# Kernel tuning notes

Measured on AMD Instinct MI355X. Metric: run time of the kernel, lower is better.

## Reference

```python
import jax, jax.numpy as jnp
import numpy as np

SEQ_LEN, N_FEAT, EMB = 512, 8, 64
HID = 2 * EMB  # 128
BATCH = 512


def _lstm_layer(x, Wih, Whh, bih, bhh):
    """Single-layer LSTM, batch_first x: [B,T,F]. PyTorch gate order i,f,g,o.
    Returns (outputs [B,T,H], final hidden [B,H])."""
    B = x.shape[0]
    H = Whh.shape[1]
    # precompute input projections for all timesteps: [B,T,4H]
    xp = jnp.einsum('btf,gf->btg', x, Wih) + bih + bhh

    def step(carry, xt):
        h, c = carry
        gates = xt + h @ Whh.T  # [B,4H]
        i, f, g, o = jnp.split(gates, 4, axis=-1)
        i = jax.nn.sigmoid(i)
        f = jax.nn.sigmoid(f)
        g = jnp.tanh(g)
        o = jax.nn.sigmoid(o)
        c = f * c + i * g
        h = o * jnp.tanh(c)
        return (h, c), h

    h0 = jnp.zeros((B, H), dtype=x.dtype)
    c0 = jnp.zeros((B, H), dtype=x.dtype)
    (hT, _), hs = jax.lax.scan(step, (h0, c0), xp.transpose(1, 0, 2))
    return hs.transpose(1, 0, 2), hT


def setup_inputs() -> dict:
    key = jax.random.key(0)
    ks = jax.random.split(key, 13)
    inp = {"x": jax.random.normal(ks[0], (BATCH, SEQ_LEN, N_FEAT), dtype=jnp.float32)}

    def mk(k, shape, fan):
        s = 1.0 / np.sqrt(fan)
        return jax.random.uniform(k, shape, dtype=jnp.float32, minval=-s, maxval=s)

    # layer 1: in=N_FEAT, hid=HID
    inp["Wih1"] = mk(ks[1], (4 * HID, N_FEAT), HID)
    inp["Whh1"] = mk(ks[2], (4 * HID, HID), HID)
    inp["bih1"] = mk(ks[3], (4 * HID,), HID)
    inp["bhh1"] = mk(ks[4], (4 * HID,), HID)
    # layer 2: in=HID, hid=HID
    inp["Wih2"] = mk(ks[5], (4 * HID, HID), HID)
    inp["Whh2"] = mk(ks[6], (4 * HID, HID), HID)
    inp["bih2"] = mk(ks[7], (4 * HID,), HID)
    inp["bhh2"] = mk(ks[8], (4 * HID,), HID)
    # layer 3: in=HID, hid=EMB
    inp["Wih3"] = mk(ks[9], (4 * EMB, HID), EMB)
    inp["Whh3"] = mk(ks[10], (4 * EMB, EMB), EMB)
    inp["bih3"] = mk(ks[11], (4 * EMB,), EMB)
    inp["bhh3"] = mk(ks[12], (4 * EMB,), EMB)
    return inp


def reference(x, Wih1, Whh1, bih1, bhh1, Wih2, Whh2, bih2, bhh2, Wih3, Whh3, bih3, bhh3):
    B = x.shape[0]
    x = x.reshape(B, SEQ_LEN, N_FEAT)
    x, _ = _lstm_layer(x, Wih1, Whh1, bih1, bhh1)
    x, _ = _lstm_layer(x, Wih2, Whh2, bih2, bhh2)
    _, hT = _lstm_layer(x, Wih3, Whh3, bih3, bhh3)
    return hT  # [B, EMB]
```

## Files before the change

kernel.cpp:

```cpp
#include <hip/hip_runtime.h>


#define DEVI __device__ __forceinline__

typedef _Float16 h4 __attribute__((ext_vector_type(4)));
typedef _Float16 h8 __attribute__((ext_vector_type(8)));
typedef float f4 __attribute__((ext_vector_type(4)));

static constexpr int T_ = 512, TC_ = 16, NC_ = T_ / TC_, RC_ = 4;
static constexpr float KS_ = -1.44269504f;
static constexpr float KG_ = -2.88539008f;

DEVI float rcpf_(float x) { return __builtin_amdgcn_rcpf(x); }
DEVI float exp2f_(float x) { return __builtin_amdgcn_exp2f(x); }

DEVI h8 cvt8s(const float* p, float s) {
    const float4 a = *reinterpret_cast<const float4*>(p);
    const float4 b = *reinterpret_cast<const float4*>(p + 4);
    return h8{(_Float16)(a.x * s), (_Float16)(a.y * s), (_Float16)(a.z * s), (_Float16)(a.w * s),
              (_Float16)(b.x * s), (_Float16)(b.y * s), (_Float16)(b.z * s), (_Float16)(b.w * s)};
}

DEVI void lds_barrier() {
    asm volatile("s_waitcnt lgkmcnt(0)\n\ts_barrier" ::: "memory");
}
DEVI int ld_flag(int* f) {
    return __hip_atomic_load(f, __ATOMIC_RELAXED, __HIP_MEMORY_SCOPE_AGENT);
}
DEVI void st_flag(int* f, int v) {
    __hip_atomic_store(f, v, __ATOMIC_RELAXED, __HIP_MEMORY_SCOPE_AGENT);
}

#define POINTWISE_PROLOG(ACC)                                                   \
    float e0[4], e1[4], e2[4], e3[4];                                           \
    _Pragma("unroll") for (int i = 0; i < 4; i++) {                             \
        e0[i] = exp2f_(ACC[0][i]);                                              \
        e1[i] = exp2f_(ACC[1][i]);                                              \
        e2[i] = exp2f_(ACC[2][i]);                                              \
        e3[i] = exp2f_(ACC[3][i]); }

#define POINTWISE_CELL(i, C, HVAR)                                              \
    const float gi = rcpf_(1.f + e0[i]), gf = rcpf_(1.f + e1[i]);               \
    const float gg = 2.f * rcpf_(1.f + e2[i]) - 1.f, go = rcpf_(1.f + e3[i]);   \
    C[i] = gf * C[i] + gi * gg;                                                 \
    const float HVAR = go * (2.f * rcpf_(1.f + exp2f_(C[i] * KG_)) - 1.f);

DEVI float gscale(int q) { return (q == 2) ? KG_ : KS_; }

DEVI void stage_L1(int tile, char* smem, const float* x, const float* Wih,
                   const float* Whh, const float* bih, const float* bhh,
                   _Float16* o1, int* c1, int* p1) {
    constexpr int H = 128, KT_H = 4, HP = H + 8;
    const int tid = threadIdx.x, lane = tid & 63, wv = tid >> 6;
    const int lr = lane & 15, lk = lane >> 4;
    const int b0 = tile * 16;
    const int jcol = wv * 16 + lr;
    _Float16 (*h_lds)[16][HP] = (_Float16 (*)[16][HP])smem;

    h8 wbh[4][KT_H], wbx[4];
    float bias[4];
#pragma unroll
    for (int q = 0; q < 4; q++) {
        const float s = gscale(q);
#pragma unroll
        for (int kt = 0; kt < KT_H; kt++)
            wbh[q][kt] = cvt8s(Whh + (size_t)(q * H + jcol) * H + kt * 32 + lk * 8, s);
        wbx[q] = (lk == 0) ? cvt8s(Wih + (size_t)(q * H + jcol) * 8, s) : h8{};
        bias[q] = (bih[q * H + jcol] + bhh[q * H + jcol]) * s;
    }
    float c[4] = {0.f, 0.f, 0.f, 0.f};
    for (int i = tid; i < 2 * 16 * HP; i += 512) ((_Float16*)smem)[i] = (_Float16)0;
    __syncthreads();

    auto load_x = [&](int t, h8& xa) {
        if (lk == 0) xa = cvt8s(x + ((size_t)(b0 + lr) * T_ + t) * 8, 1.f);
    };
    h8 xa = h8{}, xb = h8{};

#define L1_STEP(TT, CUR, XS) {                                                  \
    const int tt = (TT);                                                        \
    h8 ha[KT_H];                                                                \
    _Pragma("unroll") for (int kt = 0; kt < KT_H; kt++)                         \
        ha[kt] = *reinterpret_cast<const h8*>(&h_lds[CUR][lr][kt * 32 + lk * 8]); \
    f4 acc[4];                                                                  \
    _Pragma("unroll") for (int q = 0; q < 4; q++)                               \
        acc[q] = f4{bias[q], bias[q], bias[q], bias[q]};                        \
    _Pragma("unroll") for (int q = 0; q < 4; q++)                               \
        acc[q] = __builtin_amdgcn_mfma_f32_16x16x32_f16(XS, wbx[q], acc[q], 0, 0, 0); \
    _Pragma("unroll") for (int kt = 0; kt < KT_H; kt++)                         \
        _Pragma("unroll") for (int q = 0; q < 4; q++)                           \
            acc[q] = __builtin_amdgcn_mfma_f32_16x16x32_f16(ha[kt], wbh[q][kt], acc[q], 0, 0, 0); \
    if (tt + 2 < TC_) load_x(t0 + tt + 2, XS);                                  \
    POINTWISE_PROLOG(acc)                                                       \
    _Pragma("unroll") for (int i = 0; i < 4; i++) {                             \
        POINTWISE_CELL(i, c, h)                                                 \
        const int row = lk * 4 + i;                                             \
        h_lds[(CUR) ^ 1][row][jcol] = (_Float16)h;                              \
        o1[(((size_t)(tile * RC_ + slot) * TC_ + tt) * 16 + row) * 128 + jcol] = (_Float16)h; } }

    for (int ch = 0; ch < NC_; ch++) {
        const int slot = ch & (RC_ - 1);
        if (tid == 0) {
            while (ld_flag(c1) < ch - (RC_ - 1)) __builtin_amdgcn_s_sleep(8);
        }
        __syncthreads();
        const int t0 = ch * TC_;
        load_x(t0, xa); load_x(t0 + 1, xb);
        for (int tb = 0; tb < TC_ / 2; tb++) {
            L1_STEP(2 * tb, 0, xa) lds_barrier();
            L1_STEP(2 * tb + 1, 1, xb) lds_barrier();
        }
        asm volatile("s_waitcnt vmcnt(0)" ::: "memory");
        __syncthreads();
        if (tid == 0) { __threadfence(); st_flag(p1, ch + 1); }
    }
#undef L1_STEP
}

DEVI void stage_P2(int tile, const _Float16* o1, _Float16* xp, const float* Wih,
                   const float* bih, const float* bhh,
                   int* p1, int* c1, int* cx, int* px) {
    constexpr int H = 128;
    const int tid = threadIdx.x, lane = tid & 63, wv = tid >> 6;
    const int lr = lane & 15, lk = lane >> 4;
    const int jcol = wv * 16 + lr;

    h8 wbx[4][4];
    float pbias[4];
#pragma unroll
    for (int q = 0; q < 4; q++) {
        const float s = gscale(q);
#pragma unroll
        for (int kt = 0; kt < 4; kt++)
            wbx[q][kt] = cvt8s(Wih + (size_t)(q * H + jcol) * 128 + kt * 32 + lk * 8, s);
        pbias[q] = (bih[q * H + jcol] + bhh[q * H + jcol]) * s;
    }

    for (int ch = 0; ch < NC_; ch++) {
        const int slot = ch & (RC_ - 1);
        if (tid == 0) {
            while (ld_flag(p1) < ch + 1) __builtin_amdgcn_s_sleep(8);
            while (ld_flag(cx) < ch - (RC_ - 1)) __builtin_amdgcn_s_sleep(8);
            __threadfence();
        }
        __syncthreads();
        const size_t ib = (size_t)(tile * RC_ + slot) * TC_ * 2048;
        const size_t ob = (size_t)(tile * RC_ + slot) * TC_ * 8192;
#pragma unroll 4
        for (int t = 0; t < TC_; t++) {
            h8 af[4];
#pragma unroll
            for (int kt = 0; kt < 4; kt++)
                af[kt] = *reinterpret_cast<const h8*>(o1 + ib + (size_t)t * 2048 + lr * 128 + kt * 32 + lk * 8);
            f4 acc[4];
#pragma unroll
            for (int q = 0; q < 4; q++) acc[q] = f4{pbias[q], pbias[q], pbias[q], pbias[q]};
#pragma unroll
            for (int kt = 0; kt < 4; kt++)
#pragma unroll
                for (int q = 0; q < 4; q++)
                    acc[q] = __builtin_amdgcn_mfma_f32_16x16x32_f16(af[kt], wbx[q][kt], acc[q], 0, 0, 0);
#pragma unroll
            for (int q = 0; q < 4; q++) {
                const h4 o = h4{(_Float16)acc[q][0], (_Float16)acc[q][1],
                                (_Float16)acc[q][2], (_Float16)acc[q][3]};
                *reinterpret_cast<h4*>(xp + ob + (size_t)t * 8192 + (wv * 4 + q) * 256 + lane * 4) = o;
            }
        }
        asm volatile("s_waitcnt vmcnt(0)" ::: "memory");
        __syncthreads();
        if (tid == 0) { __threadfence(); st_flag(px, ch + 1); st_flag(c1, ch + 1); }
    }
}

DEVI void stage_L2(int tile, char* smem, const _Float16* xp, _Float16* O2,
                   const float* Whh, int* px, int* cx, int* p2) {
    constexpr int H = 128, KT_H = 4, HP = H + 8;
    const int tid = threadIdx.x, lane = tid & 63, wv = tid >> 6;
    const int lr = lane & 15, lk = lane >> 4;
    const int b0 = tile * 16;
    const int jcol = wv * 16 + lr;
    _Float16 (*h_lds)[16][HP] = (_Float16 (*)[16][HP])smem;

    h8 wbh[4][KT_H];
#pragma unroll
    for (int q = 0; q < 4; q++) {
        const float s = gscale(q);
#pragma unroll
        for (int kt = 0; kt < KT_H; kt++)
            wbh[q][kt] = cvt8s(Whh + (size_t)(q * H + jcol) * H + kt * 32 + lk * 8, s);
    }
    float c[4] = {0.f, 0.f, 0.f, 0.f};
    for (int i = tid; i < 2 * 16 * HP; i += 512) ((_Float16*)smem)[i] = (_Float16)0;
    __syncthreads();

    h4 xqa[4], xqb[4];

#define LOAD_XP(SLOT, TTL, DST) {                                               \
    const size_t base = ((size_t)(tile * RC_ + (SLOT)) * TC_ + (TTL)) * 8192 + wv * 1024 + lane * 4; \
    _Pragma("unroll") for (int q = 0; q < 4; q++)                               \
        DST[q] = *reinterpret_cast<const h4*>(xp + base + q * 256); }

#define L2_STEP(TT, CUR, XQ) {                                                  \
    const int tt = (TT); const int t = t0 + tt;                                 \
    h8 ha[KT_H];                                                                \
    _Pragma("unroll") for (int kt = 0; kt < KT_H; kt++)                         \
        ha[kt] = *reinterpret_cast<const h8*>(&h_lds[CUR][lr][kt * 32 + lk * 8]); \
    f4 acc[4];                                                                  \
    _Pragma("unroll") for (int q = 0; q < 4; q++)                               \
        acc[q] = f4{(float)XQ[q][0], (float)XQ[q][1], (float)XQ[q][2], (float)XQ[q][3]}; \
    _Pragma("unroll") for (int kt = 0; kt < KT_H; kt++)                         \
        _Pragma("unroll") for (int q = 0; q < 4; q++)                           \
            acc[q] = __builtin_amdgcn_mfma_f32_16x16x32_f16(ha[kt], wbh[q][kt], acc[q], 0, 0, 0); \
    if (tt + 2 < TC_) LOAD_XP(slot, tt + 2, XQ)                                 \
    POINTWISE_PROLOG(acc)                                                       \
    _Pragma("unroll") for (int i = 0; i < 4; i++) {                             \
        POINTWISE_CELL(i, c, h)                                                 \
        const int row = lk * 4 + i;                                             \
        h_lds[(CUR) ^ 1][row][jcol] = (_Float16)h;                              \
        O2[((size_t)t * 512 + (b0 + row)) * 128 + jcol] = (_Float16)h; } }

    for (int ch = 0; ch < NC_; ch++) {
        const int slot = ch & (RC_ - 1);
        if (tid == 0) {
            while (ld_flag(px) < ch + 1) __builtin_amdgcn_s_sleep(8);
            __threadfence();
        }
        __syncthreads();
        const int t0 = ch * TC_;
        LOAD_XP(slot, 0, xqa)
        LOAD_XP(slot, 1, xqb)
        for (int tb = 0; tb < TC_ / 2; tb++) {
            L2_STEP(2 * tb, 0, xqa) lds_barrier();
            L2_STEP(2 * tb + 1, 1, xqb) lds_barrier();
        }
        asm volatile("s_waitcnt vmcnt(0)" ::: "memory");
        __syncthreads();
        if (tid == 0) { __threadfence(); st_flag(p2, ch + 1); st_flag(cx, ch + 1); }
    }
#undef L2_STEP
#undef LOAD_XP
}

DEVI void stage_L3(int tile, char* smem, const _Float16* O2, const float* Wih,
                   const float* Whh, const float* bih, const float* bhh,
                   float* out, int* p2) {
    constexpr int H = 64, KT_H = 2, KT_X = 4, HP = H + 8;
    const int tid = threadIdx.x, lane = tid & 63, wv = tid >> 6;
    const int lr = lane & 15, lk = lane >> 4;
    const int b0 = tile * 16;
    const bool act = (wv < 4);
    const int jcol = (wv & 3) * 16 + lr;
    _Float16 (*h_lds)[16][HP] = (_Float16 (*)[16][HP])smem;

    h8 wbh[4][KT_H], wbx[4][KT_X];
    float bias[4];
    if (act) {
#pragma unroll
        for (int q = 0; q < 4; q++) {
            const float s = gscale(q);
#pragma unroll
            for (int kt = 0; kt < KT_H; kt++)
                wbh[q][kt] = cvt8s(Whh + (size_t)(q * H + jcol) * H + kt * 32 + lk * 8, s);
#pragma unroll
            for (int kt = 0; kt < KT_X; kt++)
                wbx[q][kt] = cvt8s(Wih + (size_t)(q * H + jcol) * 128 + kt * 32 + lk * 8, s);
            bias[q] = (bih[q * H + jcol] + bhh[q * H + jcol]) * s;
        }
    }
    float c[4] = {0.f, 0.f, 0.f, 0.f};
    for (int i = tid; i < 2 * 16 * HP; i += 512) ((_Float16*)smem)[i] = (_Float16)0;
    __syncthreads();

    auto load_x = [&](int t, h8* xa) {
#pragma unroll
        for (int kt = 0; kt < KT_X; kt++)
            xa[kt] = *reinterpret_cast<const h8*>(
                O2 + ((size_t)t * 512 + (b0 + lr)) * 128 + kt * 32 + lk * 8);
    };
    h8 xa[KT_X], xb[KT_X];

#define L3_STEP(TT, CUR, XS) {                                                  \
    const int tt = (TT); const int t = t0 + tt;                                 \
    if (act) {                                                                  \
        h8 ha[KT_H];                                                            \
        _Pragma("unroll") for (int kt = 0; kt < KT_H; kt++)                     \
            ha[kt] = *reinterpret_cast<const h8*>(&h_lds[CUR][lr][kt * 32 + lk * 8]); \
        f4 acc[4];                                                              \
        _Pragma("unroll") for (int q = 0; q < 4; q++)                           \
            acc[q] = f4{bias[q], bias[q], bias[q], bias[q]};                    \
        _Pragma("unroll") for (int kt = 0; kt < KT_X; kt++)                     \
            _Pragma("unroll") for (int q = 0; q < 4; q++)                       \
                acc[q] = __builtin_amdgcn_mfma_f32_16x16x32_f16(XS[kt], wbx[q][kt], acc[q], 0, 0, 0); \
        _Pragma("unroll") for (int kt = 0; kt < KT_H; kt++)                     \
            _Pragma("unroll") for (int q = 0; q < 4; q++)                       \
                acc[q] = __builtin_amdgcn_mfma_f32_16x16x32_f16(ha[kt], wbh[q][kt], acc[q], 0, 0, 0); \
        if (tt + 2 < TC_) load_x(t + 2, XS);                                    \
        POINTWISE_PROLOG(acc)                                                   \
        _Pragma("unroll") for (int i = 0; i < 4; i++) {                         \
            POINTWISE_CELL(i, c, h)                                             \
            const int row = lk * 4 + i;                                         \
            h_lds[(CUR) ^ 1][row][jcol] = (_Float16)h;                          \
            if (t == T_ - 1) out[(size_t)(b0 + row) * 64 + jcol] = h; } } }

    for (int ch = 0; ch < NC_; ch++) {
        if (tid == 0) {
            while (ld_flag(p2) < ch + 1) __builtin_amdgcn_s_sleep(8);
            __threadfence();
        }
        __syncthreads();
        const int t0 = ch * TC_;
        if (act) { load_x(t0, xa); load_x(t0 + 1, xb); }
        for (int tb = 0; tb < TC_ / 2; tb++) {
            L3_STEP(2 * tb, 0, xa) lds_barrier();
            L3_STEP(2 * tb + 1, 1, xb) lds_barrier();
        }
    }
#undef L3_STEP
}

__global__ __launch_bounds__(512, 1)
void mega_k(const float* __restrict__ x,
            const float* __restrict__ Wih1, const float* __restrict__ Whh1,
            const float* __restrict__ bih1, const float* __restrict__ bhh1,
            const float* __restrict__ Wih2, const float* __restrict__ Whh2,
            const float* __restrict__ bih2, const float* __restrict__ bhh2,
            const float* __restrict__ Wih3, const float* __restrict__ Whh3,
            const float* __restrict__ bih3, const float* __restrict__ bhh3,
            _Float16* __restrict__ o1ring, _Float16* __restrict__ xpring,
            _Float16* __restrict__ O2, float* __restrict__ out,
            int* __restrict__ flags) {
    extern __shared__ char smem[];
    const int bid = blockIdx.x;
    int* p1 = flags;
    int* c1 = flags + 32;
    int* px = flags + 64;
    int* cx = flags + 96;
    int* p2 = flags + 128;
    if (bid < 32) {
        stage_L1(bid, smem, x, Wih1, Whh1, bih1, bhh1, o1ring, c1 + bid, p1 + bid);
    } else if (bid < 64) {
        const int t = bid - 32;
        stage_P2(t, o1ring, xpring, Wih2, bih2, bhh2, p1 + t, c1 + t, cx + t, px + t);
    } else if (bid < 96) {
        const int t = bid - 64;
        stage_L2(t, smem, xpring, O2, Whh2, px + t, cx + t, p2 + t);
    } else {
        const int t = bid - 96;
        stage_L3(t, smem, O2, Wih3, Whh3, bih3, bhh3, out, p2 + t);
    }
}

__global__ void zero_flags_k(int* flags) {
    if (threadIdx.x < 160)
        __hip_atomic_store(flags + threadIdx.x, 0, __ATOMIC_RELAXED,
                           __HIP_MEMORY_SCOPE_AGENT);
}

extern "C" void kernel_launch(void* const* d_in, const int* in_sizes, int n_in,
                              void* d_out, int out_size, void* d_ws, size_t ws_size,
                              hipStream_t stream) {
    const float* x = (const float*)d_in[0];
    float* out = (float*)d_out;

    char* ws = (char*)d_ws;
    _Float16* o1ring = (_Float16*)ws;
    _Float16* xpring = (_Float16*)(ws + (size_t)8388608);
    _Float16* O2     = (_Float16*)(ws + (size_t)41943040);
    int* flags       = (int*)(ws + (size_t)109051904);
    (void)ws_size; (void)in_sizes; (void)n_in; (void)out_size;

    zero_flags_k<<<1, 192, 0, stream>>>(flags);
    mega_k<<<128, 512, 8704, stream>>>(
        x,
        (const float*)d_in[1], (const float*)d_in[2], (const float*)d_in[3], (const float*)d_in[4],
        (const float*)d_in[5], (const float*)d_in[6], (const float*)d_in[7], (const float*)d_in[8],
        (const float*)d_in[9], (const float*)d_in[10], (const float*)d_in[11], (const float*)d_in[12],
        o1ring, xpring, O2, out, flags);
}
```

Before: 712.2 us.

## Process two batch tiles per block in recurrent LSTM stages

Each L1, L2 and L3 block now handles two 16-row batch tiles instead of one. L1 and L2 interleave two independent recurrences so each tile's MFMA chain can hide the other's latency. L3 puts the second tile on the four previously idle waves. The grid shrinks from 128 to 80 blocks, shared memory per block doubles, and the O2 layout changes from time-major to batch-major. The cost is a longer serial step per block and higher register pressure.

```diff
diff --git a/kernel.cpp b/kernel.cpp
--- a/kernel.cpp
+++ b/kernel.cpp
@@ -31,31 +31,30 @@
     __hip_atomic_store(f, v, __ATOMIC_RELAXED, __HIP_MEMORY_SCOPE_AGENT);
 }
 
-#define POINTWISE_PROLOG(ACC)                                                   \
+DEVI float gscale(int q) { return (q == 2) ? KG_ : KS_; }
+
+#define PW_PROLOG(A)                                                            \
     float e0[4], e1[4], e2[4], e3[4];                                           \
     _Pragma("unroll") for (int i = 0; i < 4; i++) {                             \
-        e0[i] = exp2f_(ACC[0][i]);                                              \
-        e1[i] = exp2f_(ACC[1][i]);                                              \
-        e2[i] = exp2f_(ACC[2][i]);                                              \
-        e3[i] = exp2f_(ACC[3][i]); }
-
-#define POINTWISE_CELL(i, C, HVAR)                                              \
+        e0[i] = exp2f_(A[0][i]); e1[i] = exp2f_(A[1][i]);                       \
+        e2[i] = exp2f_(A[2][i]); e3[i] = exp2f_(A[3][i]); }
+
+#define PW_CELL(i, C, HVAR)                                                     \
     const float gi = rcpf_(1.f + e0[i]), gf = rcpf_(1.f + e1[i]);               \
     const float gg = 2.f * rcpf_(1.f + e2[i]) - 1.f, go = rcpf_(1.f + e3[i]);   \
     C[i] = gf * C[i] + gi * gg;                                                 \
     const float HVAR = go * (2.f * rcpf_(1.f + exp2f_(C[i] * KG_)) - 1.f);
 
-DEVI float gscale(int q) { return (q == 2) ? KG_ : KS_; }
-
-DEVI void stage_L1(int tile, char* smem, const float* x, const float* Wih,
+DEVI void stage_L1(int tA, int tB, char* smem, const float* x, const float* Wih,
                    const float* Whh, const float* bih, const float* bhh,
                    _Float16* o1, int* c1, int* p1) {
     constexpr int H = 128, KT_H = 4, HP = H + 8;
     const int tid = threadIdx.x, lane = tid & 63, wv = tid >> 6;
     const int lr = lane & 15, lk = lane >> 4;
-    const int b0 = tile * 16;
+    const int b0A = tA * 16, b0B = tB * 16;
     const int jcol = wv * 16 + lr;
-    _Float16 (*h_lds)[16][HP] = (_Float16 (*)[16][HP])smem;
+    _Float16 (*hA)[16][HP] = (_Float16 (*)[16][HP])smem;
+    _Float16 (*hB)[16][HP] = (_Float16 (*)[16][HP])(smem + 2 * 16 * HP * 2);
 
     h8 wbh[4][KT_H], wbx[4];
     float bias[4];
@@ -68,53 +67,74 @@
         wbx[q] = (lk == 0) ? cvt8s(Wih + (size_t)(q * H + jcol) * 8, s) : h8{};
         bias[q] = (bih[q * H + jcol] + bhh[q * H + jcol]) * s;
     }
-    float c[4] = {0.f, 0.f, 0.f, 0.f};
-    for (int i = tid; i < 2 * 16 * HP; i += 512) ((_Float16*)smem)[i] = (_Float16)0;
+    float cA[4] = {0.f, 0.f, 0.f, 0.f}, cB[4] = {0.f, 0.f, 0.f, 0.f};
+    for (int i = tid; i < 2 * 2 * 16 * HP; i += 512) ((_Float16*)smem)[i] = (_Float16)0;
     __syncthreads();
 
-    auto load_x = [&](int t, h8& xa) {
+    auto load_x = [&](int b0, int t, h8& xa) {
         if (lk == 0) xa = cvt8s(x + ((size_t)(b0 + lr) * T_ + t) * 8, 1.f);
     };
-    h8 xa = h8{}, xb = h8{};
-
-#define L1_STEP(TT, CUR, XS) {                                                  \
+    h8 xAe = h8{}, xAo = h8{}, xBe = h8{}, xBo = h8{};
+
+#define L1S(TT, CUR, XA, XB) {                                                  \
     const int tt = (TT);                                                        \
-    h8 ha[KT_H];                                                                \
-    _Pragma("unroll") for (int kt = 0; kt < KT_H; kt++)                         \
-        ha[kt] = *reinterpret_cast<const h8*>(&h_lds[CUR][lr][kt * 32 + lk * 8]); \
-    f4 acc[4];                                                                  \
-    _Pragma("unroll") for (int q = 0; q < 4; q++)                               \
-        acc[q] = f4{bias[q], bias[q], bias[q], bias[q]};                        \
-    _Pragma("unroll") for (int q = 0; q < 4; q++)                               \
-        acc[q] = __builtin_amdgcn_mfma_f32_16x16x32_f16(XS, wbx[q], acc[q], 0, 0, 0); \
-    _Pragma("unroll") for (int kt = 0; kt < KT_H; kt++)                         \
-        _Pragma("unroll") for (int q = 0; q < 4; q++)                           \
-            acc[q] = __builtin_amdgcn_mfma_f32_16x16x32_f16(ha[kt], wbh[q][kt], acc[q], 0, 0, 0); \
-    if (tt + 2 < TC_) load_x(t0 + tt + 2, XS);                                  \
-    POINTWISE_PROLOG(acc)                                                       \
-    _Pragma("unroll") for (int i = 0; i < 4; i++) {                             \
-        POINTWISE_CELL(i, c, h)                                                 \
-        const int row = lk * 4 + i;                                             \
-        h_lds[(CUR) ^ 1][row][jcol] = (_Float16)h;                              \
-        o1[(((size_t)(tile * RC_ + slot) * TC_ + tt) * 16 + row) * 128 + jcol] = (_Float16)h; } }
+    h8 haA[KT_H], haB[KT_H];                                                    \
+    _Pragma("unroll") for (int kt = 0; kt < KT_H; kt++) {                       \
+        haA[kt] = *reinterpret_cast<const h8*>(&hA[CUR][lr][kt * 32 + lk * 8]); \
+        haB[kt] = *reinterpret_cast<const h8*>(&hB[CUR][lr][kt * 32 + lk * 8]); } \
+    f4 aA[4], aB[4];                                                            \
+    _Pragma("unroll") for (int q = 0; q < 4; q++) {                             \
+        aA[q] = f4{bias[q], bias[q], bias[q], bias[q]};                         \
+        aB[q] = f4{bias[q], bias[q], bias[q], bias[q]}; }                       \
+    _Pragma("unroll") for (int q = 0; q < 4; q++) {                             \
+        aA[q] = __builtin_amdgcn_mfma_f32_16x16x32_f16(XA, wbx[q], aA[q], 0, 0, 0); \
+        aB[q] = __builtin_amdgcn_mfma_f32_16x16x32_f16(XB, wbx[q], aB[q], 0, 0, 0); } \
+    _Pragma("unroll") for (int kt = 0; kt < KT_H; kt++)                         \
+        _Pragma("unroll") for (int q = 0; q < 4; q++)                           \
+            aA[q] = __builtin_amdgcn_mfma_f32_16x16x32_f16(haA[kt], wbh[q][kt], aA[q], 0, 0, 0); \
+    _Pragma("unroll") for (int kt = 0; kt < KT_H; kt++)                         \
+        _Pragma("unroll") for (int q = 0; q < 4; q++)                           \
+            aB[q] = __builtin_amdgcn_mfma_f32_16x16x32_f16(haB[kt], wbh[q][kt], aB[q], 0, 0, 0); \
+    if (tt + 2 < TC_) { load_x(b0A, t0 + tt + 2, XA); load_x(b0B, t0 + tt + 2, XB); } \
+    {                                                                           \
+        PW_PROLOG(aA)                                                           \
+        _Pragma("unroll") for (int i = 0; i < 4; i++) {                         \
+            PW_CELL(i, cA, h)                                                   \
+            const int row = lk * 4 + i;                                         \
+            hA[(CUR) ^ 1][row][jcol] = (_Float16)h;                             \
+            o1[(((size_t)(tA * RC_ + slot) * TC_ + tt) * 16 + row) * 128 + jcol] = (_Float16)h; } \
+    }                                                                           \
+    {                                                                           \
+        PW_PROLOG(aB)                                                           \
+        _Pragma("unroll") for (int i = 0; i < 4; i++) {                         \
+            PW_CELL(i, cB, h)                                                   \
+            const int row = lk * 4 + i;                                         \
+            hB[(CUR) ^ 1][row][jcol] = (_Float16)h;                             \
+            o1[(((size_t)(tB * RC_ + slot) * TC_ + tt) * 16 + row) * 128 + jcol] = (_Float16)h; } \
+    } }
 
     for (int ch = 0; ch < NC_; ch++) {
         const int slot = ch & (RC_ - 1);
         if (tid == 0) {
-            while (ld_flag(c1) < ch - (RC_ - 1)) __builtin_amdgcn_s_sleep(8);
+            while (ld_flag(c1 + tA) < ch - (RC_ - 1)) __builtin_amdgcn_s_sleep(8);
+            while (ld_flag(c1 + tB) < ch - (RC_ - 1)) __builtin_amdgcn_s_sleep(8);
         }
         __syncthreads();
         const int t0 = ch * TC_;
-        load_x(t0, xa); load_x(t0 + 1, xb);
+        load_x(b0A, t0, xAe); load_x(b0A, t0 + 1, xAo);
+        load_x(b0B, t0, xBe); load_x(b0B, t0 + 1, xBo);
         for (int tb = 0; tb < TC_ / 2; tb++) {
-            L1_STEP(2 * tb, 0, xa) lds_barrier();
-            L1_STEP(2 * tb + 1, 1, xb) lds_barrier();
+            L1S(2 * tb, 0, xAe, xBe) lds_barrier();
+            L1S(2 * tb + 1, 1, xAo, xBo) lds_barrier();
         }
         asm volatile("s_waitcnt vmcnt(0)" ::: "memory");
         __syncthreads();
-        if (tid == 0) { __threadfence(); st_flag(p1, ch + 1); }
-    }
-#undef L1_STEP
+        if (tid == 0) {
+            __threadfence();
+            st_flag(p1 + tA, ch + 1); st_flag(p1 + tB, ch + 1);
+        }
+    }
+#undef L1S
 }
 
 DEVI void stage_P2(int tile, const _Float16* o1, _Float16* xp, const float* Wih,
@@ -173,14 +193,15 @@
     }
 }
 
-DEVI void stage_L2(int tile, char* smem, const _Float16* xp, _Float16* O2,
+DEVI void stage_L2(int tA, int tB, char* smem, const _Float16* xp, _Float16* O2,
                    const float* Whh, int* px, int* cx, int* p2) {
     constexpr int H = 128, KT_H = 4, HP = H + 8;
     const int tid = threadIdx.x, lane = tid & 63, wv = tid >> 6;
     const int lr = lane & 15, lk = lane >> 4;
-    const int b0 = tile * 16;
+    const int b0A = tA * 16, b0B = tB * 16;
     const int jcol = wv * 16 + lr;
-    _Float16 (*h_lds)[16][HP] = (_Float16 (*)[16][HP])smem;
+    _Float16 (*hA)[16][HP] = (_Float16 (*)[16][HP])smem;
+    _Float16 (*hB)[16][HP] = (_Float16 (*)[16][HP])(smem + 2 * 16 * HP * 2);
 
     h8 wbh[4][KT_H];
 #pragma unroll
@@ -190,133 +211,155 @@
         for (int kt = 0; kt < KT_H; kt++)
             wbh[q][kt] = cvt8s(Whh + (size_t)(q * H + jcol) * H + kt * 32 + lk * 8, s);
     }
-    float c[4] = {0.f, 0.f, 0.f, 0.f};
-    for (int i = tid; i < 2 * 16 * HP; i += 512) ((_Float16*)smem)[i] = (_Float16)0;
+    float cA[4] = {0.f, 0.f, 0.f, 0.f}, cB[4] = {0.f, 0.f, 0.f, 0.f};
+    for (int i = tid; i < 2 * 2 * 16 * HP; i += 512) ((_Float16*)smem)[i] = (_Float16)0;
     __syncthreads();
 
-    h4 xqa[4], xqb[4];
-
-#define LOAD_XP(SLOT, TTL, DST) {                                               \
-    const size_t base = ((size_t)(tile * RC_ + (SLOT)) * TC_ + (TTL)) * 8192 + wv * 1024 + lane * 4; \
+    h4 xqAe[4], xqAo[4], xqBe[4], xqBo[4];
+
+#define LOAD_XP(TI, SLOT, TTL, DST) {                                           \
+    const size_t base = ((size_t)((TI) * RC_ + (SLOT)) * TC_ + (TTL)) * 8192 + wv * 1024 + lane * 4; \
     _Pragma("unroll") for (int q = 0; q < 4; q++)                               \
         DST[q] = *reinterpret_cast<const h4*>(xp + base + q * 256); }
 
-#define L2_STEP(TT, CUR, XQ) {                                                  \
+#define L2S(TT, CUR, XQA, XQB) {                                                \
     const int tt = (TT); const int t = t0 + tt;                                 \
-    h8 ha[KT_H];                                                                \
-    _Pragma("unroll") for (int kt = 0; kt < KT_H; kt++)                         \
-        ha[kt] = *reinterpret_cast<const h8*>(&h_lds[CUR][lr][kt * 32 + lk * 8]); \
-    f4 acc[4];                                                                  \
-    _Pragma("unroll") for (int q = 0; q < 4; q++)                               \
-        acc[q] = f4{(float)XQ[q][0], (float)XQ[q][1], (float)XQ[q][2], (float)XQ[q][3]}; \
-    _Pragma("unroll") for (int kt = 0; kt < KT_H; kt++)                         \
-        _Pragma("unroll") for (int q = 0; q < 4; q++)                           \
-            acc[q] = __builtin_amdgcn_mfma_f32_16x16x32_f16(ha[kt], wbh[q][kt], acc[q], 0, 0, 0); \
-    if (tt + 2 < TC_) LOAD_XP(slot, tt + 2, XQ)                                 \
-    POINTWISE_PROLOG(acc)                                                       \
-    _Pragma("unroll") for (int i = 0; i < 4; i++) {                             \
-        POINTWISE_CELL(i, c, h)                                                 \
-        const int row = lk * 4 + i;                                             \
-        h_lds[(CUR) ^ 1][row][jcol] = (_Float16)h;                              \
-        O2[((size_t)t * 512 + (b0 + row)) * 128 + jcol] = (_Float16)h; } }
+    h8 haA[KT_H], haB[KT_H];                                                    \
+    _Pragma("unroll") for (int kt = 0; kt < KT_H; kt++) {                       \
+        haA[kt] = *reinterpret_cast<const h8*>(&hA[CUR][lr][kt * 32 + lk * 8]); \
+        haB[kt] = *reinterpret_cast<const h8*>(&hB[CUR][lr][kt * 32 + lk * 8]); } \
+    f4 aA[4], aB[4];                                                            \
+    _Pragma("unroll") for (int q = 0; q < 4; q++) {                             \
+        aA[q] = f4{(float)XQA[q][0], (float)XQA[q][1], (float)XQA[q][2], (float)XQA[q][3]}; \
+        aB[q] = f4{(float)XQB[q][0], (float)XQB[q][1], (float)XQB[q][2], (float)XQB[q][3]}; } \
+    _Pragma("unroll") for (int kt = 0; kt < KT_H; kt++)                         \
+        _Pragma("unroll") for (int q = 0; q < 4; q++)                           \
+            aA[q] = __builtin_amdgcn_mfma_f32_16x16x32_f16(haA[kt], wbh[q][kt], aA[q], 0, 0, 0); \
+    _Pragma("unroll") for (int kt = 0; kt < KT_H; kt++)                         \
+        _Pragma("unroll") for (int q = 0; q < 4; q++)                           \
+            aB[q] = __builtin_amdgcn_mfma_f32_16x16x32_f16(haB[kt], wbh[q][kt], aB[q], 0, 0, 0); \
+    if (tt + 2 < TC_) { LOAD_XP(tA, slot, tt + 2, XQA) LOAD_XP(tB, slot, tt + 2, XQB) } \
+    {                                                                           \
+        PW_PROLOG(aA)                                                           \
+        _Pragma("unroll") for (int i = 0; i < 4; i++) {                         \
+            PW_CELL(i, cA, h)                                                   \
+            const int row = lk * 4 + i;                                         \
+            hA[(CUR) ^ 1][row][jcol] = (_Float16)h;                             \
+            O2[((size_t)(b0A + row) * T_ + t) * 128 + jcol] = (_Float16)h; }    \
+    }                                                                           \
+    {                                                                           \
+        PW_PROLOG(aB)                                                           \
+        _Pragma("unroll") for (int i = 0; i < 4; i++) {                         \
+            PW_CELL(i, cB, h)                                                   \
+            const int row = lk * 4 + i;                                         \
+            hB[(CUR) ^ 1][row][jcol] = (_Float16)h;                             \
+            O2[((size_t)(b0B + row) * T_ + t) * 128 + jcol] = (_Float16)h; }    \
+    } }
 
     for (int ch = 0; ch < NC_; ch++) {
         const int slot = ch & (RC_ - 1);
         if (tid == 0) {
-            while (ld_flag(px) < ch + 1) __builtin_amdgcn_s_sleep(8);
+            while (ld_flag(px + tA) < ch + 1) __builtin_amdgcn_s_sleep(8);
+            while (ld_flag(px + tB) < ch + 1) __builtin_amdgcn_s_sleep(8);
             __threadfence();
         }
         __syncthreads();
         const int t0 = ch * TC_;
-        LOAD_XP(slot, 0, xqa)
-        LOAD_XP(slot, 1, xqb)
+        LOAD_XP(tA, slot, 0, xqAe) LOAD_XP(tA, slot, 1, xqAo)
+        LOAD_XP(tB, slot, 0, xqBe) LOAD_XP(tB, slot, 1, xqBo)
         for (int tb = 0; tb < TC_ / 2; tb++) {
-            L2_STEP(2 * tb, 0, xqa) lds_barrier();
-            L2_STEP(2 * tb + 1, 1, xqb) lds_barrier();
+            L2S(2 * tb, 0, xqAe, xqBe) lds_barrier();
+            L2S(2 * tb + 1, 1, xqAo, xqBo) lds_barrier();
         }
         asm volatile("s_waitcnt vmcnt(0)" ::: "memory");
         __syncthreads();
-        if (tid == 0) { __threadfence(); st_flag(p2, ch + 1); st_flag(cx, ch + 1); }
-    }
-#undef L2_STEP
+        if (tid == 0) {
+            __threadfence();
+            st_flag(p2 + tA, ch + 1); st_flag(p2 + tB, ch + 1);
+            st_flag(cx + tA, ch + 1); st_flag(cx + tB, ch + 1);
+        }
+    }
+#undef L2S
 #undef LOAD_XP
 }
 
-DEVI void stage_L3(int tile, char* smem, const _Float16* O2, const float* Wih,
+DEVI void stage_L3(int tA, int tB, char* smem, const _Float16* O2, const float* Wih,
                    const float* Whh, const float* bih, const float* bhh,
                    float* out, int* p2) {
     constexpr int H = 64, KT_H = 2, KT_X = 4, HP = H + 8;
     const int tid = threadIdx.x, lane = tid & 63, wv = tid >> 6;
     const int lr = lane & 15, lk = lane >> 4;
-    const int b0 = tile * 16;
-    const bool act = (wv < 4);
-    const int jcol = (wv & 3) * 16 + lr;
-    _Float16 (*h_lds)[16][HP] = (_Float16 (*)[16][HP])smem;
+    const int myTile = (wv >= 4) ? tB : tA;
+    const int b0 = myTile * 16;
+    const int jg = wv & 3;
+    const int jcol = jg * 16 + lr;
+    _Float16 (*h_lds)[16][HP] =
+        (_Float16 (*)[16][HP])(smem + (size_t)(wv >= 4 ? 2 * 16 * HP * 2 : 0));
 
     h8 wbh[4][KT_H], wbx[4][KT_X];
     float bias[4];
-    if (act) {
-#pragma unroll
-        for (int q = 0; q < 4; q++) {
-            const float s = gscale(q);
-#pragma unroll
-            for (int kt = 0; kt < KT_H; kt++)
-                wbh[q][kt] = cvt8s(Whh + (size_t)(q * H + jcol) * H + kt * 32 + lk * 8, s);
-#pragma unroll
-            for (int kt = 0; kt < KT_X; kt++)
-                wbx[q][kt] = cvt8s(Wih + (size_t)(q * H + jcol) * 128 + kt * 32 + lk * 8, s);
-            bias[q] = (bih[q * H + jcol] + bhh[q * H + jcol]) * s;
-        }
+#pragma unroll
+    for (int q = 0; q < 4; q++) {
+        const float s = gscale(q);
+#pragma unroll
+        for (int kt = 0; kt < KT_H; kt++)
+            wbh[q][kt] = cvt8s(Whh + (size_t)(q * H + jcol) * H + kt * 32 + lk * 8, s);
+#pragma unroll
+        for (int kt = 0; kt < KT_X; kt++)
+            wbx[q][kt] = cvt8s(Wih + (size_t)(q * H + jcol) * 128 + kt * 32 + lk * 8, s);
+        bias[q] = (bih[q * H + jcol] + bhh[q * H + jcol]) * s;
     }
     float c[4] = {0.f, 0.f, 0.f, 0.f};
-    for (int i = tid; i < 2 * 16 * HP; i += 512) ((_Float16*)smem)[i] = (_Float16)0;
+    for (int i = tid; i < 2 * 2 * 16 * HP; i += 512) ((_Float16*)smem)[i] = (_Float16)0;
     __syncthreads();
 
     auto load_x = [&](int t, h8* xa) {
 #pragma unroll
         for (int kt = 0; kt < KT_X; kt++)
             xa[kt] = *reinterpret_cast<const h8*>(
-                O2 + ((size_t)t * 512 + (b0 + lr)) * 128 + kt * 32 + lk * 8);
+                O2 + ((size_t)(b0 + lr) * T_ + t) * 128 + kt * 32 + lk * 8);
     };
     h8 xa[KT_X], xb[KT_X];
 
-#define L3_STEP(TT, CUR, XS) {                                                  \
+#define L3S(TT, CUR, XS) {                                                      \
     const int tt = (TT); const int t = t0 + tt;                                 \
-    if (act) {                                                                  \
-        h8 ha[KT_H];                                                            \
-        _Pragma("unroll") for (int kt = 0; kt < KT_H; kt++)                     \
-            ha[kt] = *reinterpret_cast<const h8*>(&h_lds[CUR][lr][kt * 32 + lk * 8]); \
-        f4 acc[4];                                                              \
-        _Pragma("unroll") for (int q = 0; q < 4; q++)                           \
-            acc[q] = f4{bias[q], bias[q], bias[q], bias[q]};                    \
-        _Pragma("unroll") for (int kt = 0; kt < KT_X; kt++)                     \
-            _Pragma("unroll") for (int q = 0; q < 4; q++)                       \
-                acc[q] = __builtin_amdgcn_mfma_f32_16x16x32_f16(XS[kt], wbx[q][kt], acc[q], 0, 0, 0); \
-        _Pragma("unroll") for (int kt = 0; kt < KT_H; kt++)                     \
-            _Pragma("unroll") for (int q = 0; q < 4; q++)                       \
-                acc[q] = __builtin_amdgcn_mfma_f32_16x16x32_f16(ha[kt], wbh[q][kt], acc[q], 0, 0, 0); \
-        if (tt + 2 < TC_) load_x(t + 2, XS);                                    \
-        POINTWISE_PROLOG(acc)                                                   \
+    h8 ha[KT_H];                                                                \
+    _Pragma("unroll") for (int kt = 0; kt < KT_H; kt++)                         \
+        ha[kt] = *reinterpret_cast<const h8*>(&h_lds[CUR][lr][kt * 32 + lk * 8]); \
+    f4 acc[4];                                                                  \
+    _Pragma("unroll") for (int q = 0; q < 4; q++)                               \
+        acc[q] = f4{bias[q], bias[q], bias[q], bias[q]};                        \
+    _Pragma("unroll") for (int kt = 0; kt < KT_X; kt++)                         \
+        _Pragma("unroll") for (int q = 0; q < 4; q++)                           \
+            acc[q] = __builtin_amdgcn_mfma_f32_16x16x32_f16(XS[kt], wbx[q][kt], acc[q], 0, 0, 0); \
+    _Pragma("unroll") for (int kt = 0; kt < KT_H; kt++)                         \
+        _Pragma("unroll") for (int q = 0; q < 4; q++)                           \
+            acc[q] = __builtin_amdgcn_mfma_f32_16x16x32_f16(ha[kt], wbh[q][kt], acc[q], 0, 0, 0); \
+    if (tt + 2 < TC_) load_x(t + 2, XS);                                        \
+    {                                                                           \
+        PW_PROLOG(acc)                                                          \
         _Pragma("unroll") for (int i = 0; i < 4; i++) {                         \
-            POINTWISE_CELL(i, c, h)                                             \
+            PW_CELL(i, c, h)                                                    \
             const int row = lk * 4 + i;                                         \
             h_lds[(CUR) ^ 1][row][jcol] = (_Float16)h;                          \
-            if (t == T_ - 1) out[(size_t)(b0 + row) * 64 + jcol] = h; } } }
+            if (t == T_ - 1) out[(size_t)(b0 + row) * 64 + jcol] = h; }         \
+    } }
 
     for (int ch = 0; ch < NC_; ch++) {
         if (tid == 0) {
-            while (ld_flag(p2) < ch + 1) __builtin_amdgcn_s_sleep(8);
+            while (ld_flag(p2 + tA) < ch + 1) __builtin_amdgcn_s_sleep(8);
+            while (ld_flag(p2 + tB) < ch + 1) __builtin_amdgcn_s_sleep(8);
             __threadfence();
         }
         __syncthreads();
         const int t0 = ch * TC_;
-        if (act) { load_x(t0, xa); load_x(t0 + 1, xb); }
+        load_x(t0, xa); load_x(t0 + 1, xb);
         for (int tb = 0; tb < TC_ / 2; tb++) {
-            L3_STEP(2 * tb, 0, xa) lds_barrier();
-            L3_STEP(2 * tb + 1, 1, xb) lds_barrier();
-        }
-    }
-#undef L3_STEP
+            L3S(2 * tb, 0, xa) lds_barrier();
+            L3S(2 * tb + 1, 1, xb) lds_barrier();
+        }
+    }
+#undef L3S
 }
 
 __global__ __launch_bounds__(512, 1)
@@ -337,17 +380,17 @@
     int* px = flags + 64;
     int* cx = flags + 96;
     int* p2 = flags + 128;
-    if (bid < 32) {
-        stage_L1(bid, smem, x, Wih1, Whh1, bih1, bhh1, o1ring, c1 + bid, p1 + bid);
+    if (bid < 16) {
+        stage_L1(2 * bid, 2 * bid + 1, smem, x, Wih1, Whh1, bih1, bhh1, o1ring, c1, p1);
+    } else if (bid < 48) {
+        const int t = bid - 16;
+        stage_P2(t, o1ring, xpring, Wih2, bih2, bhh2, p1 + t, c1 + t, cx + t, px + t);
     } else if (bid < 64) {
-        const int t = bid - 32;
-        stage_P2(t, o1ring, xpring, Wih2, bih2, bhh2, p1 + t, c1 + t, cx + t, px + t);
-    } else if (bid < 96) {
-        const int t = bid - 64;
-        stage_L2(t, smem, xpring, O2, Whh2, px + t, cx + t, p2 + t);
+        const int p = bid - 48;
+        stage_L2(2 * p, 2 * p + 1, smem, xpring, O2, Whh2, px, cx, p2);
     } else {
-        const int t = bid - 96;
-        stage_L3(t, smem, O2, Wih3, Whh3, bih3, bhh3, out, p2 + t);
+        const int p = bid - 64;
+        stage_L3(2 * p, 2 * p + 1, smem, O2, Wih3, Whh3, bih3, bhh3, out, p2);
     }
 }
 
@@ -371,7 +414,7 @@
     (void)ws_size; (void)in_sizes; (void)n_in; (void)out_size;
 
     zero_flags_k<<<1, 192, 0, stream>>>(flags);
-    mega_k<<<128, 512, 8704, stream>>>(
+    mega_k<<<80, 512, 17408, stream>>>(
         x,
         (const float*)d_in[1], (const float*)d_in[2], (const float*)d_in[3], (const float*)d_in[4],
         (const float*)d_in[5], (const float*)d_in[6], (const float*)d_in[7], (const float*)d_in[8],
```

Measured after the change: 1.063 ms. 1.49x slower.
